# Kernel optimization log

Measured on AMD Instinct MI355X. Metric: run time of the kernel, lower is better.

Reference implementation:

```python
import jax, jax.numpy as jnp
import numpy as np

B, N, D = 512, 100000, 64
TAU = 1e-4            # gumbel-softmax temperature from source
SIM_RATIO = 0.5       # similarity_ratio init kwarg
COS_EPS = 1e-6


def setup_inputs() -> dict:
    key = jax.random.key(0)
    k1, k2, k3, k4, k5 = jax.random.split(key, 5)
    need_replace = jax.random.randint(k1, (B, 2), 0, N, dtype=jnp.int64) if jax.config.jax_enable_x64 else jax.random.randint(k1, (B, 2), 0, N, dtype=jnp.int32)
    union_feature = jax.random.normal(k2, (B, 2 * D), dtype=jnp.float32)
    all_items = jax.random.normal(k3, (N, D), dtype=jnp.float32) * 0.1
    W = jax.random.normal(k4, (D, 2 * D), dtype=jnp.float32) * 0.05
    b = jax.random.normal(k5, (D,), dtype=jnp.float32) * 0.01
    return {"need_replace": need_replace, "union_feature": union_feature,
            "all_items": all_items, "W": W, "b": b}


def _cosine(a, b):
    # torch.nn.CosineSimilarity(dim=1, eps=1e-6): dot / max(||a||*||b||, eps)
    dot = jnp.sum(a * b, axis=1)
    na = jnp.linalg.norm(a, axis=1)
    nb = jnp.linalg.norm(b, axis=1)
    return dot / jnp.maximum(na * nb, COS_EPS)


def reference(need_replace, union_feature, all_items, W, b):
    item_ids = need_replace[:, 1]
    items_emb = all_items[item_ids]                      # [B, D]
    uif = union_feature @ W.T + b                        # [B, D] (nn.Linear)
    score = uif @ all_items.T                            # [B, N]

    # gumbel_softmax(tau=1e-4, hard=True), training branch
    g = jax.random.gumbel(jax.random.key(42), score.shape, dtype=score.dtype)
    y_soft = jax.nn.softmax((score + g) / TAU, axis=-1)  # [B, N]
    idx = jnp.argmax(y_soft, axis=-1)                    # [B]
    y_hard = jax.nn.one_hot(idx, N, dtype=score.dtype)
    P = y_hard + y_soft - jax.lax.stop_gradient(y_soft)  # straight-through hard one-hot

    item_sequence = jnp.arange(N, dtype=score.dtype)[None, :]
    replaceable_items = jnp.sum(P * item_sequence, axis=-1).astype(jnp.int32)
    replaceable_feat = P @ all_items                     # [B, D]

    sim = _cosine(items_emb, replaceable_feat)
    sim = (sim + 1.0) / 2.0                              # regularize_similarity
    labels = jnp.full((B,), SIM_RATIO, dtype=sim.dtype)
    similarity_loss = jnp.mean((sim - labels) ** 2)      # SimilarityMarginLoss (assumed MSE-to-margin)
    return replaceable_items, replaceable_feat, similarity_loss, jnp.mean(sim)
```

## Files before the change

### kernel.cpp

```cpp
#include <hip/hip_runtime.h>
#include <cstdint>

#define NITEMS   100000
#define BROWS    512
#define DDIM     64
#define S_BLOCKS 391
#define IPB      256
#define NCHUNKS  782
#define FB_Y     16

typedef __attribute__((ext_vector_type(8)))  short  bf16x8;
typedef __attribute__((ext_vector_type(16))) float  f32x16;
typedef unsigned long long u64;
typedef uint32_t u32;

__device__ __forceinline__ u32 threefry_0_42_xor(u32 e) {
    const u32 K1 = 42u;
    const u32 K2 = 0x1BD11BDAu ^ 42u;
    u32 x0 = 0u;
    u32 x1 = e + K1;
#define TFR(r) { x0 += x1; x1 = (x1 << (r)) | (x1 >> (32 - (r))); x1 ^= x0; }
    TFR(13) TFR(15) TFR(26) TFR(6)
    x0 += K1;  x1 += K2 + 1u;
    TFR(17) TFR(29) TFR(16) TFR(24)
    x0 += K2;  x1 += 2u;
    TFR(13) TFR(15) TFR(26) TFR(6)
    x1 += K1 + 3u;
    TFR(17) TFR(29) TFR(16) TFR(24)
    x0 += K1;  x1 += K2 + 4u;
    TFR(13) TFR(15) TFR(26) TFR(6)
    x0 += K2;  x1 += 5u;
#undef TFR
    return x0 ^ x1;
}

__device__ __forceinline__ float gumbel_from_bits(u32 b) {
    float f = __uint_as_float((b >> 9) | 0x3F800000u) - 1.0f;
    f = fmaxf(f, 1.17549435e-38f);
    return -logf(-logf(f));
}

__device__ __forceinline__ u32 order_map(float v) {
    u32 x = __float_as_uint(v);
    return (x & 0x80000000u) ? ~x : (x | 0x80000000u);
}
__device__ __forceinline__ float unpack_val(u64 p) {
    u32 x = (u32)(p >> 32);
    u32 f = (x & 0x80000000u) ? (x & 0x7FFFFFFFu) : ~x;
    return __uint_as_float(f);
}

__device__ __forceinline__ short f32_to_bf16_rne(float f) {
    u32 b = __float_as_uint(f);
    u32 r = (b + 0x7FFFu + ((b >> 16) & 1u)) >> 16;
    return (short)r;
}
__device__ __forceinline__ float bf16_to_f32(short h) {
    return __uint_as_float(((u32)(uint16_t)h) << 16);
}

__global__ void uif_kernel(const float* __restrict__ UF, const float* __restrict__ W,
                           const float* __restrict__ bias, float* __restrict__ uif,
                           float* __restrict__ unorm, u32* __restrict__ amax_bits,
                           int* __restrict__ cnt) {
    int b = blockIdx.x, d = threadIdx.x;
    if (b == 0 && d == 0) { *cnt = 0; *amax_bits = 0u; }
    const float* w = W + d * 128;
    const float* u = UF + b * 128;
    float s = 0.f;
    for (int k = 0; k < 128; k++) s = fmaf(u[k], w[k], s);
    s += bias[d];
    uif[b * 64 + d] = s;
    float q = s * s;
#pragma unroll
    for (int o = 32; o >= 1; o >>= 1) q += __shfl_xor(q, o);
    if (d == 0) unorm[b] = sqrtf(q);
}

__global__ void anorm_kernel(const float* __restrict__ A, u32* __restrict__ amax_bits) {
    int item = blockIdx.x * 256 + threadIdx.x;
    float q = 0.f;
    if (item < NITEMS) {
        const float4* r = (const float4*)(A + (size_t)item * DDIM);
#pragma unroll
        for (int k = 0; k < 16; k++) {
            float4 x = r[k];
            q = fmaf(x.x, x.x, q); q = fmaf(x.y, x.y, q);
            q = fmaf(x.z, x.z, q); q = fmaf(x.w, x.w, q);
        }
    }
    float n = sqrtf(q);
#pragma unroll
    for (int o = 32; o >= 1; o >>= 1) n = fmaxf(n, __shfl_xor(n, o));
    if ((threadIdx.x & 63) == 0) atomicMax(amax_bits, __float_as_uint(n));
}

__global__ __launch_bounds__(256, 3) void phase1_kernel(
        const float* __restrict__ A, const float* __restrict__ uif,
        u64* __restrict__ wsT1, float* __restrict__ wsT2) {
    __shared__ bf16x8 sh_ah[4 * 64];
    __shared__ bf16x8 sh_al[4 * 64];
    const int tid  = threadIdx.x;
    const int lane = tid & 63;
    const int wv   = tid >> 6;
    const int rg   = blockIdx.y;
    const int sb   = blockIdx.x;
    const int itembase = sb * IPB;
    const int ntiles = min(8, (NITEMS - itembase + 31) >> 5);
    const int row   = rg * 128 + wv * 32 + (lane & 31);
    const int khalf = (lane >> 5) * 8;

    bf16x8 uh[4], ul[4];
#pragma unroll
    for (int s = 0; s < 4; s++) {
        const float* src = uif + row * 64 + khalf + 16 * s;
        float4 v0 = *(const float4*)src;
        float4 v1 = *(const float4*)(src + 4);
        float vv[8] = {v0.x, v0.y, v0.z, v0.w, v1.x, v1.y, v1.z, v1.w};
        bf16x8 h, l2;
#pragma unroll
        for (int j = 0; j < 8; j++) {
            short hh = f32_to_bf16_rne(vv[j]);
            float r  = vv[j] - bf16_to_f32(hh);
            h[j] = hh; l2[j] = f32_to_bf16_rne(r);
        }
        uh[s] = h; ul[s] = l2;
    }

    u64 t1p = 0ull; float t1f = -3.0e38f, t2f = -3.0e38f;
    const u32 rowbase_e = (u32)row * (u32)NITEMS;

    for (int t = 0; t < ntiles; t++) {
        const int tb = itembase + t * 32;
        __syncthreads();
        {
            const int i = tid >> 3, c = tid & 7;
            const float* src = A + (size_t)(tb + i) * 64 + 8 * c;
            float4 v0 = *(const float4*)src;
            float4 v1 = *(const float4*)(src + 4);
            float vv[8] = {v0.x, v0.y, v0.z, v0.w, v1.x, v1.y, v1.z, v1.w};
            bf16x8 h, l2;
#pragma unroll
            for (int j = 0; j < 8; j++) {
                short hh = f32_to_bf16_rne(vv[j]);
                float r  = vv[j] - bf16_to_f32(hh);
                h[j] = hh; l2[j] = f32_to_bf16_rne(r);
            }
            const int dst = (c >> 1) * 64 + (i & 31) + 32 * (c & 1);
            sh_ah[dst] = h; sh_al[dst] = l2;
        }
        __syncthreads();

        f32x16 acc;
#pragma unroll
        for (int z = 0; z < 16; z++) acc[z] = 0.0f;
#pragma unroll
        for (int s = 0; s < 4; s++) {
            bf16x8 ah = sh_ah[s * 64 + lane];
            bf16x8 al = sh_al[s * 64 + lane];
            acc = __builtin_amdgcn_mfma_f32_32x32x16_bf16(ah, uh[s], acc, 0, 0, 0);
            acc = __builtin_amdgcn_mfma_f32_32x32x16_bf16(al, uh[s], acc, 0, 0, 0);
            acc = __builtin_amdgcn_mfma_f32_32x32x16_bf16(ah, ul[s], acc, 0, 0, 0);
        }

        const int ib4 = tb + 4 * (lane >> 5);
#pragma unroll
        for (int i = 0; i < 16; i++) {
            const int il   = (i & 3) + 8 * (i >> 2);
            const int item = ib4 + il;
            u32 rb  = threefry_0_42_xor(rowbase_e + (u32)item);
            float g = gumbel_from_bits(rb);
            float v = acc[i] + g;
            if (v > t1f) {
                t2f = t1f; t1f = v;
                t1p = ((u64)order_map(v) << 32) | (u32)(~(u32)item);
            } else {
                t2f = fmaxf(t2f, v);
            }
        }
    }

    {
        u64   op = __shfl_xor(t1p, 32);
        float of = __shfl_xor(t1f, 32);
        float o2 = __shfl_xor(t2f, 32);
        if (op > t1p) { t2f = fmaxf(t1f, o2); t1p = op; t1f = of; }
        else          { t2f = fmaxf(t2f, of); }
    }
    if (lane < 32) {
        wsT1[(size_t)row * S_BLOCKS + sb] = t1p;
        wsT2[(size_t)row * S_BLOCKS + sb] = t2f;
    }
}

__global__ void merge_kernel(const u64* __restrict__ wsT1, const float* __restrict__ wsT2,
                             const float* __restrict__ unorm, const u32* __restrict__ amax_bits,
                             u64* __restrict__ packed, int* __restrict__ rowlist,
                             int* __restrict__ cnt) {
    const int row = blockIdx.x, t = threadIdx.x;
    u64 p1 = 0ull; float f1 = -3.0e38f, f2 = -3.0e38f;
    for (int sbk = t; sbk < S_BLOCKS; sbk += 64) {
        u64 ep   = wsT1[(size_t)row * S_BLOCKS + sbk];
        float e2 = wsT2[(size_t)row * S_BLOCKS + sbk];
        if (ep > p1) { f2 = fmaxf(f1, e2); p1 = ep; f1 = unpack_val(ep); }
        else         { f2 = fmaxf(f2, unpack_val(ep)); }
    }
#pragma unroll
    for (int off = 1; off < 64; off <<= 1) {
        u64   op  = __shfl_xor(p1, off);
        float of1 = __shfl_xor(f1, off);
        float of2 = __shfl_xor(f2, off);
        if (op > p1) { f2 = fmaxf(f1, of2); p1 = op; f1 = of1; }
        else         { f2 = fmaxf(f2, of1); }
    }
    if (t == 0) {
        float Amax = __uint_as_float(*amax_bits);
        float E = 1.5e-4f * unorm[row] * Amax + 3.0e-5f;
        if ((f1 - f2) > 2.0f * E) {
            packed[row] = p1;
        } else {
            packed[row] = 0ull;
            rowlist[atomicAdd(cnt, 1)] = row;
        }
    }
}

__global__ void fallback_kernel(const float* __restrict__ A, const float* __restrict__ uif,
                                const int* __restrict__ rowlist, const int* __restrict__ cnt,
                                u64* __restrict__ packed) {
    __shared__ float As[128 * 65];
    __shared__ float Us[64];
    const int t  = threadIdx.x;
    const int c  = blockIdx.x;
    const int n0 = c * 128;
    const int nitem = min(128, NITEMS - n0);
    const int total = *cnt;
    if ((int)blockIdx.y >= total) return;

    if (t < nitem) {
        const float4* src = (const float4*)(A + (size_t)(n0 + t) * 64);
#pragma unroll
        for (int k4 = 0; k4 < 16; k4++) {
            float4 x = src[k4];
            As[t * 65 + 4 * k4 + 0] = x.x; As[t * 65 + 4 * k4 + 1] = x.y;
            As[t * 65 + 4 * k4 + 2] = x.z; As[t * 65 + 4 * k4 + 3] = x.w;
        }
    }
    for (int li = blockIdx.y; li < total; li += FB_Y) {
        const int row = rowlist[li];
        __syncthreads();
        if (t < 64) Us[t] = uif[row * 64 + t];
        __syncthreads();
        u64 pk = 0ull;
        if (t < nitem) {
            const int item = n0 + t;
            u32 rb  = threefry_0_42_xor((u32)row * (u32)NITEMS + (u32)item);
            float g = gumbel_from_bits(rb);
            float s0 = 0.f, s1 = 0.f;
#pragma unroll
            for (int k8 = 0; k8 < 64; k8 += 8) {
                s0 = fmaf(As[t * 65 + k8 + 0], Us[k8 + 0], s0);
                s0 = fmaf(As[t * 65 + k8 + 1], Us[k8 + 1], s0);
                s0 = fmaf(As[t * 65 + k8 + 2], Us[k8 + 2], s0);
                s0 = fmaf(As[t * 65 + k8 + 3], Us[k8 + 3], s0);
                s1 = fmaf(As[t * 65 + k8 + 4], Us[k8 + 4], s1);
                s1 = fmaf(As[t * 65 + k8 + 5], Us[k8 + 5], s1);
                s1 = fmaf(As[t * 65 + k8 + 6], Us[k8 + 6], s1);
                s1 = fmaf(As[t * 65 + k8 + 7], Us[k8 + 7], s1);
            }
            float v = (s0 + s1) + g;
            pk = ((u64)order_map(v) << 32) | (u32)(~(u32)item);
        }
#pragma unroll
        for (int off = 1; off < 64; off <<= 1) {
            u64 o = __shfl_xor(pk, off);
            pk = (o > pk) ? o : pk;
        }
        if ((t & 63) == 0) atomicMax(&packed[row], pk);
        __syncthreads();
    }
}

__global__ void finalize_kernel(const u64* __restrict__ packed, const float* __restrict__ A,
                                const int* __restrict__ need_replace,
                                float* __restrict__ out, float* __restrict__ sims) {
    int b = blockIdx.x, lane = threadIdx.x;
    u64 pk = packed[b];
    int idx = (int)(~(u32)(pk & 0xFFFFFFFFull));
    float fr = A[(size_t)idx * DDIM + lane];
    out[512 + b * DDIM + lane] = fr;
    int   item = need_replace[2 * b + 1];
    float fa   = A[(size_t)item * DDIM + lane];
    float dot = fa * fr, na2 = fa * fa, nb2 = fr * fr;
#pragma unroll
    for (int o = 32; o >= 1; o >>= 1) {
        dot += __shfl_down(dot, o);
        na2 += __shfl_down(na2, o);
        nb2 += __shfl_down(nb2, o);
    }
    if (lane == 0) {
        out[b] = (float)idx;
        float denom = fmaxf(sqrtf(na2) * sqrtf(nb2), 1e-6f);
        sims[b] = (dot / denom + 1.0f) * 0.5f;
    }
}

__global__ void loss_kernel(const float* __restrict__ sims, float* __restrict__ out) {
    __shared__ float shL[8], shS[8];
    int t = threadIdx.x;
    float s = sims[t];
    float d = s - 0.5f;
    float l = d * d;
#pragma unroll
    for (int o = 32; o >= 1; o >>= 1) { l += __shfl_down(l, o); s += __shfl_down(s, o); }
    int w = t >> 6;
    if ((t & 63) == 0) { shL[w] = l; shS[w] = s; }
    __syncthreads();
    if (t == 0) {
        float L = 0.f, S = 0.f;
        for (int i = 0; i < 8; i++) { L += shL[i]; S += shS[i]; }
        out[512 + 512 * DDIM]     = L / 512.0f;
        out[512 + 512 * DDIM + 1] = S / 512.0f;
    }
}

extern "C" void kernel_launch(void* const* d_in, const int* in_sizes, int n_in,
                              void* d_out, int out_size, void* d_ws, size_t ws_size,
                              hipStream_t stream) {
    (void)in_sizes; (void)n_in; (void)out_size; (void)ws_size;
    const int*   need_replace = (const int*)d_in[0];
    const float* UF           = (const float*)d_in[1];
    const float* A            = (const float*)d_in[2];
    const float* W            = (const float*)d_in[3];
    const float* bias         = (const float*)d_in[4];
    float* out = (float*)d_out;

    char* ws = (char*)d_ws;
    u64*   wsT1    = (u64*)  (ws);
    float* wsT2    = (float*)(ws + 1601536);
    float* uif     = (float*)(ws + 2402304);
    u64*   packed  = (u64*)  (ws + 2533376);
    float* unorm   = (float*)(ws + 2537472);
    float* sims    = (float*)(ws + 2539520);
    int*   rowlist = (int*)  (ws + 2541568);
    u32*   amax    = (u32*)  (ws + 2543616);
    int*   cnt     = (int*)  (ws + 2543620);

    uif_kernel<<<BROWS, 64, 0, stream>>>(UF, W, bias, uif, unorm, amax, cnt);
    anorm_kernel<<<S_BLOCKS, 256, 0, stream>>>(A, amax);
    phase1_kernel<<<dim3(S_BLOCKS, 4), 256, 0, stream>>>(A, uif, wsT1, wsT2);
    merge_kernel<<<BROWS, 64, 0, stream>>>(wsT1, wsT2, unorm, amax, packed, rowlist, cnt);
    fallback_kernel<<<dim3(NCHUNKS, FB_Y), 128, 0, stream>>>(A, uif, rowlist, cnt, packed);
    finalize_kernel<<<BROWS, 64, 0, stream>>>(packed, A, need_replace, out, sims);
    loss_kernel<<<1, 512, 0, stream>>>(sims, out);
}
```

Before: 294.7 us.

## Skip Gumbel evaluation for low-noise items and fuse small kernels

```diff
diff --git a/kernel.cpp b/kernel.cpp
--- a/kernel.cpp
+++ b/kernel.cpp
@@ -7,7 +7,14 @@
 #define S_BLOCKS 391
 #define IPB      256
 #define NCHUNKS  782
-#define FB_Y     16
+#define FB_Y     8
+#define OUT_FEAT 512
+#define OUT_LOSS (512 + 512 * 64)
+#define OUT_MSIM (OUT_LOSS + 1)
+
+#define BITS23_T   8367841u
+#define BITS_RAW_T 4284334592u
+#define G_TE       6.001f
 
 typedef __attribute__((ext_vector_type(8)))  short  bf16x8;
 typedef __attribute__((ext_vector_type(16))) float  f32x16;
@@ -49,7 +56,6 @@
     u32 f = (x & 0x80000000u) ? (x & 0x7FFFFFFFu) : ~x;
     return __uint_as_float(f);
 }
-
 __device__ __forceinline__ short f32_to_bf16_rne(float f) {
     u32 b = __float_as_uint(f);
     u32 r = (b + 0x7FFFu + ((b >> 16) & 1u)) >> 16;
@@ -59,45 +65,47 @@
     return __uint_as_float(((u32)(uint16_t)h) << 16);
 }
 
-__global__ void uif_kernel(const float* __restrict__ UF, const float* __restrict__ W,
-                           const float* __restrict__ bias, float* __restrict__ uif,
-                           float* __restrict__ unorm, u32* __restrict__ amax_bits,
-                           int* __restrict__ cnt) {
-    int b = blockIdx.x, d = threadIdx.x;
-    if (b == 0 && d == 0) { *cnt = 0; *amax_bits = 0u; }
-    const float* w = W + d * 128;
-    const float* u = UF + b * 128;
-    float s = 0.f;
-    for (int k = 0; k < 128; k++) s = fmaf(u[k], w[k], s);
-    s += bias[d];
-    uif[b * 64 + d] = s;
-    float q = s * s;
-#pragma unroll
-    for (int o = 32; o >= 1; o >>= 1) q += __shfl_xor(q, o);
-    if (d == 0) unorm[b] = sqrtf(q);
-}
-
-__global__ void anorm_kernel(const float* __restrict__ A, u32* __restrict__ amax_bits) {
-    int item = blockIdx.x * 256 + threadIdx.x;
-    float q = 0.f;
-    if (item < NITEMS) {
-        const float4* r = (const float4*)(A + (size_t)item * DDIM);
-#pragma unroll
-        for (int k = 0; k < 16; k++) {
-            float4 x = r[k];
-            q = fmaf(x.x, x.x, q); q = fmaf(x.y, x.y, q);
-            q = fmaf(x.z, x.z, q); q = fmaf(x.w, x.w, q);
-        }
-    }
-    float n = sqrtf(q);
-#pragma unroll
-    for (int o = 32; o >= 1; o >>= 1) n = fmaxf(n, __shfl_xor(n, o));
-    if ((threadIdx.x & 63) == 0) atomicMax(amax_bits, __float_as_uint(n));
-}
-
-__global__ __launch_bounds__(256, 3) void phase1_kernel(
+__global__ void prep_kernel(const float* __restrict__ UF, const float* __restrict__ W,
+                            const float* __restrict__ bias, const float* __restrict__ A,
+                            float* __restrict__ uif, float* __restrict__ unorm,
+                            float* __restrict__ wsAM4, int* __restrict__ cnt) {
+    const int t = threadIdx.x, b = blockIdx.x;
+    if (b == 0 && t == 0) *cnt = 0;
+    if (b < 128) {
+        const int row = b * 4 + (t >> 6);
+        const int d   = t & 63;
+        const float* w = W + d * 128;
+        const float* u = UF + row * 128;
+        float s = 0.f;
+        for (int k = 0; k < 128; k++) s = fmaf(u[k], w[k], s);
+        s += bias[d];
+        uif[row * 64 + d] = s;
+        float q = s * s;
+#pragma unroll
+        for (int o = 32; o >= 1; o >>= 1) q += __shfl_xor(q, o);
+        if (d == 0) unorm[row] = sqrtf(q);
+    } else {
+        const int item = (b - 128) * 256 + t;
+        float q = 0.f;
+        if (item < NITEMS) {
+            const float4* r = (const float4*)(A + (size_t)item * DDIM);
+#pragma unroll
+            for (int k = 0; k < 16; k++) {
+                float4 x = r[k];
+                q = fmaf(x.x, x.x, q); q = fmaf(x.y, x.y, q);
+                q = fmaf(x.z, x.z, q); q = fmaf(x.w, x.w, q);
+            }
+        }
+        float n = sqrtf(q);
+#pragma unroll
+        for (int o = 32; o >= 1; o >>= 1) n = fmaxf(n, __shfl_xor(n, o));
+        if ((t & 63) == 0) wsAM4[(b - 128) * 4 + (t >> 6)] = n;
+    }
+}
+
+__global__ __launch_bounds__(256, 4) void phase1_kernel(
         const float* __restrict__ A, const float* __restrict__ uif,
-        u64* __restrict__ wsT1, float* __restrict__ wsT2) {
+        u64* __restrict__ wsT1, float* __restrict__ wsB) {
     __shared__ bf16x8 sh_ah[4 * 64];
     __shared__ bf16x8 sh_al[4 * 64];
     const int tid  = threadIdx.x;
@@ -127,15 +135,19 @@
         uh[s] = h; ul[s] = l2;
     }
 
-    u64 t1p = 0ull; float t1f = -3.0e38f, t2f = -3.0e38f;
+    u64 t1p = 0ull; float t1f = -3.0e38f, t2f = -3.0e38f, sm = -3.0e38f;
     const u32 rowbase_e = (u32)row * (u32)NITEMS;
+
+    const int s_i   = tid & 31;
+    const int s_c   = tid >> 5;
+    const int s_dst = (s_c >> 1) * 64 + s_i + 32 * (s_c & 1);
+    const float* s_srcbase = A + (size_t)s_i * 64 + 8 * s_c;
 
     for (int t = 0; t < ntiles; t++) {
         const int tb = itembase + t * 32;
         __syncthreads();
         {
-            const int i = tid >> 3, c = tid & 7;
-            const float* src = A + (size_t)(tb + i) * 64 + 8 * c;
+            const float* src = s_srcbase + (size_t)tb * 64;
             float4 v0 = *(const float4*)src;
             float4 v1 = *(const float4*)(src + 4);
             float vv[8] = {v0.x, v0.y, v0.z, v0.w, v1.x, v1.y, v1.z, v1.w};
@@ -146,8 +158,7 @@
                 float r  = vv[j] - bf16_to_f32(hh);
                 h[j] = hh; l2[j] = f32_to_bf16_rne(r);
             }
-            const int dst = (c >> 1) * 64 + (i & 31) + 32 * (c & 1);
-            sh_ah[dst] = h; sh_al[dst] = l2;
+            sh_ah[s_dst] = h; sh_al[s_dst] = l2;
         }
         __syncthreads();
 
@@ -169,54 +180,60 @@
             const int il   = (i & 3) + 8 * (i >> 2);
             const int item = ib4 + il;
             u32 rb  = threefry_0_42_xor(rowbase_e + (u32)item);
-            float g = gumbel_from_bits(rb);
-            float v = acc[i] + g;
-            if (v > t1f) {
-                t2f = t1f; t1f = v;
-                t1p = ((u64)order_map(v) << 32) | (u32)(~(u32)item);
-            } else {
-                t2f = fmaxf(t2f, v);
+            float s = acc[i];
+            sm = fmaxf(sm, s);
+            if (rb >= BITS_RAW_T) {
+                float g = gumbel_from_bits(rb);
+                float v = s + g;
+                if (v > t1f) {
+                    t2f = t1f; t1f = v;
+                    t1p = ((u64)order_map(v) << 32) | (u32)(~(u32)item);
+                } else t2f = fmaxf(t2f, v);
             }
         }
     }
 
+    float bnd = fmaxf(t2f, sm + G_TE);
     {
         u64   op = __shfl_xor(t1p, 32);
         float of = __shfl_xor(t1f, 32);
-        float o2 = __shfl_xor(t2f, 32);
-        if (op > t1p) { t2f = fmaxf(t1f, o2); t1p = op; t1f = of; }
-        else          { t2f = fmaxf(t2f, of); }
+        float ob = __shfl_xor(bnd, 32);
+        if (op > t1p) { bnd = fmaxf(fmaxf(bnd, ob), t1f); t1p = op; t1f = of; }
+        else          { bnd = fmaxf(fmaxf(bnd, ob), of); }
     }
     if (lane < 32) {
         wsT1[(size_t)row * S_BLOCKS + sb] = t1p;
-        wsT2[(size_t)row * S_BLOCKS + sb] = t2f;
-    }
-}
-
-__global__ void merge_kernel(const u64* __restrict__ wsT1, const float* __restrict__ wsT2,
-                             const float* __restrict__ unorm, const u32* __restrict__ amax_bits,
+        wsB [(size_t)row * S_BLOCKS + sb] = bnd;
+    }
+}
+
+__global__ void merge_kernel(const u64* __restrict__ wsT1, const float* __restrict__ wsB,
+                             const float* __restrict__ wsAM4, const float* __restrict__ unorm,
                              u64* __restrict__ packed, int* __restrict__ rowlist,
-                             int* __restrict__ cnt) {
+                             int* __restrict__ cnt, float* __restrict__ out) {
     const int row = blockIdx.x, t = threadIdx.x;
+    if (row == 0 && t == 0) { out[OUT_LOSS] = 0.f; out[OUT_MSIM] = 0.f; }
+    float am = 0.f;
+    for (int i = t; i < S_BLOCKS * 4; i += 64) am = fmaxf(am, wsAM4[i]);
     u64 p1 = 0ull; float f1 = -3.0e38f, f2 = -3.0e38f;
     for (int sbk = t; sbk < S_BLOCKS; sbk += 64) {
-        u64 ep   = wsT1[(size_t)row * S_BLOCKS + sbk];
-        float e2 = wsT2[(size_t)row * S_BLOCKS + sbk];
-        if (ep > p1) { f2 = fmaxf(f1, e2); p1 = ep; f1 = unpack_val(ep); }
-        else         { f2 = fmaxf(f2, unpack_val(ep)); }
+        u64   ep = wsT1[(size_t)row * S_BLOCKS + sbk];
+        float e2 = wsB [(size_t)row * S_BLOCKS + sbk];
+        if (ep > p1) { f2 = fmaxf(fmaxf(f1, e2), f2); p1 = ep; f1 = unpack_val(ep); }
+        else         { float v = unpack_val(ep); f2 = fmaxf(f2, fmaxf(v, e2)); }
     }
 #pragma unroll
     for (int off = 1; off < 64; off <<= 1) {
         u64   op  = __shfl_xor(p1, off);
         float of1 = __shfl_xor(f1, off);
         float of2 = __shfl_xor(f2, off);
-        if (op > p1) { f2 = fmaxf(f1, of2); p1 = op; f1 = of1; }
-        else         { f2 = fmaxf(f2, of1); }
+        am = fmaxf(am, __shfl_xor(am, off));
+        if (op > p1) { f2 = fmaxf(fmaxf(f1, of2), f2); p1 = op; f1 = of1; }
+        else         { f2 = fmaxf(f2, fmaxf(of1, of2)); }
     }
     if (t == 0) {
-        float Amax = __uint_as_float(*amax_bits);
-        float E = 1.5e-4f * unorm[row] * Amax + 3.0e-5f;
-        if ((f1 - f2) > 2.0f * E) {
+        float E = 1.5e-4f * unorm[row] * am + 3.0e-5f;
+        if (f1 - f2 > 2.0f * E) {
             packed[row] = p1;
         } else {
             packed[row] = 0ull;
@@ -281,14 +298,13 @@
     }
 }
 
-__global__ void finalize_kernel(const u64* __restrict__ packed, const float* __restrict__ A,
-                                const int* __restrict__ need_replace,
-                                float* __restrict__ out, float* __restrict__ sims) {
+__global__ void resolve_kernel(const u64* __restrict__ packed, const float* __restrict__ A,
+                               const int* __restrict__ need_replace, float* __restrict__ out) {
     int b = blockIdx.x, lane = threadIdx.x;
     u64 pk = packed[b];
     int idx = (int)(~(u32)(pk & 0xFFFFFFFFull));
     float fr = A[(size_t)idx * DDIM + lane];
-    out[512 + b * DDIM + lane] = fr;
+    out[OUT_FEAT + b * DDIM + lane] = fr;
     int   item = need_replace[2 * b + 1];
     float fa   = A[(size_t)item * DDIM + lane];
     float dot = fa * fr, na2 = fa * fa, nb2 = fr * fr;
@@ -301,26 +317,10 @@
     if (lane == 0) {
         out[b] = (float)idx;
         float denom = fmaxf(sqrtf(na2) * sqrtf(nb2), 1e-6f);
-        sims[b] = (dot / denom + 1.0f) * 0.5f;
-    }
-}
-
-__global__ void loss_kernel(const float* __restrict__ sims, float* __restrict__ out) {
-    __shared__ float shL[8], shS[8];
-    int t = threadIdx.x;
-    float s = sims[t];
-    float d = s - 0.5f;
-    float l = d * d;
-#pragma unroll
-    for (int o = 32; o >= 1; o >>= 1) { l += __shfl_down(l, o); s += __shfl_down(s, o); }
-    int w = t >> 6;
-    if ((t & 63) == 0) { shL[w] = l; shS[w] = s; }
-    __syncthreads();
-    if (t == 0) {
-        float L = 0.f, S = 0.f;
-        for (int i = 0; i < 8; i++) { L += shL[i]; S += shS[i]; }
-        out[512 + 512 * DDIM]     = L / 512.0f;
-        out[512 + 512 * DDIM + 1] = S / 512.0f;
+        float sim = (dot / denom + 1.0f) * 0.5f;
+        float d = sim - 0.5f;
+        atomicAdd(&out[OUT_LOSS], d * d * (1.0f / 512.0f));
+        atomicAdd(&out[OUT_MSIM], sim * (1.0f / 512.0f));
     }
 }
 
@@ -337,20 +337,17 @@
 
     char* ws = (char*)d_ws;
     u64*   wsT1    = (u64*)  (ws);
-    float* wsT2    = (float*)(ws + 1601536);
+    float* wsB     = (float*)(ws + 1601536);
     float* uif     = (float*)(ws + 2402304);
     u64*   packed  = (u64*)  (ws + 2533376);
     float* unorm   = (float*)(ws + 2537472);
-    float* sims    = (float*)(ws + 2539520);
-    int*   rowlist = (int*)  (ws + 2541568);
-    u32*   amax    = (u32*)  (ws + 2543616);
-    int*   cnt     = (int*)  (ws + 2543620);
-
-    uif_kernel<<<BROWS, 64, 0, stream>>>(UF, W, bias, uif, unorm, amax, cnt);
-    anorm_kernel<<<S_BLOCKS, 256, 0, stream>>>(A, amax);
-    phase1_kernel<<<dim3(S_BLOCKS, 4), 256, 0, stream>>>(A, uif, wsT1, wsT2);
-    merge_kernel<<<BROWS, 64, 0, stream>>>(wsT1, wsT2, unorm, amax, packed, rowlist, cnt);
+    float* wsAM4   = (float*)(ws + 2539520);
+    int*   rowlist = (int*)  (ws + 2545776);
+    int*   cnt     = (int*)  (ws + 2547824);
+
+    prep_kernel<<<519, 256, 0, stream>>>(UF, W, bias, A, uif, unorm, wsAM4, cnt);
+    phase1_kernel<<<dim3(S_BLOCKS, 4), 256, 0, stream>>>(A, uif, wsT1, wsB);
+    merge_kernel<<<BROWS, 64, 0, stream>>>(wsT1, wsB, wsAM4, unorm, packed, rowlist, cnt, out);
     fallback_kernel<<<dim3(NCHUNKS, FB_Y), 128, 0, stream>>>(A, uif, rowlist, cnt, packed);
-    finalize_kernel<<<BROWS, 64, 0, stream>>>(packed, A, need_replace, out, sims);
-    loss_kernel<<<1, 512, 0, stream>>>(sims, out);
-}
+    resolve_kernel<<<BROWS, 64, 0, stream>>>(packed, A, need_replace, out);
+}
```

Result: faster. 259.3 us (-12.0%).
